# Kernel tuning notes

Hardware: AMD Instinct MI355X
Metric: run time of the kernel (lower is better)

## Reference

```python
import jax, jax.numpy as jnp
import numpy as np
from jax import lax

DN = ('NHWC', 'HWIO', 'NHWC')

def _conv(x, k, b, stride=1):
    return lax.conv_general_dilated(x, k, (stride, stride), 'SAME', dimension_numbers=DN) + b

def _tconv(x, k, b):
    return lax.conv_transpose(x, k, (2, 2), 'SAME', dimension_numbers=DN) + b


def setup_inputs() -> dict:
    key = jax.random.key(0)
    ks = jax.random.split(key, 32)
    ki = iter(ks)
    def w(shape, scale=0.05):
        return (jax.random.normal(next(ki), shape, dtype=jnp.float32) * scale)
    inp = {}
    inp['x'] = jax.random.uniform(next(ki), (8, 128, 128, 3), dtype=jnp.float32)
    # encoder
    inp['k1'],  inp['b1']  = w((11, 11, 3, 32)),   jnp.zeros((32,), jnp.float32)
    inp['k1c'], inp['b1c'] = w((3, 3, 32, 32)),    jnp.zeros((32,), jnp.float32)
    inp['k2'],  inp['b2']  = w((11, 11, 32, 64)),  jnp.zeros((64,), jnp.float32)
    inp['k2c'], inp['b2c'] = w((3, 3, 64, 64)),    jnp.zeros((64,), jnp.float32)
    inp['k3'],  inp['b3']  = w((11, 11, 64, 128)), jnp.zeros((128,), jnp.float32)
    inp['k3c'], inp['b3c'] = w((3, 3, 128, 128)),  jnp.zeros((128,), jnp.float32)
    # codebook (codebookSize=256, latent dim 128)
    inp['codebook'] = w((256, 128), 0.1)
    # decoder
    inp['tk1'],  inp['tb1']  = w((5, 5, 128, 64)), jnp.zeros((64,), jnp.float32)
    inp['tk1c'], inp['tb1c'] = w((3, 3, 64, 64)),  jnp.zeros((64,), jnp.float32)
    inp['tk2'],  inp['tb2']  = w((5, 5, 64, 32)),  jnp.zeros((32,), jnp.float32)
    inp['tk2c'], inp['tb2c'] = w((3, 3, 32, 32)),  jnp.zeros((32,), jnp.float32)
    inp['tk3'],  inp['tb3']  = w((5, 5, 32, 32)),  jnp.zeros((32,), jnp.float32)
    inp['tk3c'], inp['tb3c'] = w((3, 3, 32, 3)),   jnp.zeros((3,), jnp.float32)
    return inp


def reference(x, k1, b1, k1c, b1c, k2, b2, k2c, b2c, k3, b3, k3c, b3c,
              codebook, tk1, tb1, tk1c, tb1c, tk2, tb2, tk2c, tb2c,
              tk3, tb3, tk3c, tb3c):
    act = jax.nn.silu  # flax.nnx.swish
    # encoder
    d1 = act(_conv(x, k1, b1, 2))
    d1 = act(_conv(d1, k1c, b1c, 1))
    d2 = act(_conv(d1, k2, b2, 2))
    d2 = act(_conv(d2, k2c, b2c, 1))
    d3 = act(_conv(d2, k3, b3, 2))
    d3 = _conv(d3, k3c, b3c, 1)               # [B, H/8, W/8, 128]
    # vector quantization: squared L2 to each codebook entry
    lat = d3.reshape(-1, 1, 128)              # [N, 1, 128]
    eu_dis = jnp.sum((lat - codebook[None]) ** 2, axis=-1)   # [N, 256]
    idx = jnp.argmin(eu_dis, axis=-1)         # [N]
    quantized = jnp.take(codebook, idx, axis=0).reshape(d3.shape)
    # straight-through estimator
    replaced = lax.stop_gradient(quantized - d3) + d3
    # decoder
    d4 = act(_tconv(replaced, tk1, tb1))
    d4 = act(_conv(d4, tk1c, tb1c, 1))
    d5 = act(_tconv(d4, tk2, tb2))
    d5 = act(_conv(d5, tk2c, tb2c, 1))
    d6 = act(_tconv(d5, tk3, tb3))
    out = _conv(d6, tk3c, tb3c, 1)            # [B, H, W, 3]
    return out
```

## Files before the change

### kernel.cpp

```cpp
#include <hip/hip_runtime.h>

#define DI __device__ __forceinline__
DI float silu_f(float x){ return x * (1.0f/(1.0f+__expf(-x))); }

template<int X> struct LOG2 { static constexpr int v = 1 + LOG2<X/2>::v; };
template<> struct LOG2<1> { static constexpr int v = 0; };

template<int KH,int KW,int STRIDE,int PAD,int CIN,int COUT,int NPIX,
         bool ACT,bool BIAS,int G,int CS,int TOW>
__global__ __launch_bounds__(256) void conv_k(
    const float* __restrict__ in, const float* __restrict__ w,
    const float* __restrict__ bias, float* __restrict__ out,
    int N,int H,int W,int OH,int OW)
{
  constexpr int CLEN = CIN/G;
  constexpr int COB  = COUT/CS;
  constexpr int COQ  = COB/4;
  constexpr int GSH  = LOG2<G>::v;
  constexpr int CSH  = LOG2<CS>::v;
  constexpr int TAPF = CLEN*COB;
  constexpr bool SALL = (KH*KW*TAPF*4) <= 47*1024;
  constexpr int NTAP = SALL ? KH*KW : KW;
  static_assert(CLEN==3 || (CLEN%4)==0, "ci");
  static_assert(TOW==0 || (!SALL && NPIX==1), "tow");
  __shared__ float sw[NTAP*TAPF];
  constexpr int SPAN = (TOW>0) ? (TOW-1)*STRIDE + KW : 1;
  constexpr int ROWS = (TOW>0) ? (256/COQ)/TOW : 1;
  constexpr int CQ4  = (TOW>0) ? CLEN/4 : 1;
  __shared__ float si[(TOW>0) ? ROWS*CQ4*SPAN*4 : 1];

  const int g  = blockIdx.x & (G-1);
  const int cs = (blockIdx.x >> GSH) & (CS-1);
  const int bx = blockIdx.x >> (GSH+CSH);
  const int total = N*OH*OW;
  if (G>1) out += (size_t)g * total * COUT;
  const int ci_off  = g*CLEN;
  const int co_base = cs*COB;

  int idx = bx*256 + (int)threadIdx.x;
  int cq = idx % COQ;
  int pg = idx / COQ;
  int co = cq*4;
  int gco = co_base + co;
  int p0 = pg*NPIX;

  float acc[NPIX][4] = {};
  int iy0[NPIX], ix0[NPIX]; const float* base[NPIX]; bool pv[NPIX];
#pragma unroll
  for (int t=0;t<NPIX;t++){
    int p=p0+t; pv[t]=(p<total); int pp=pv[t]?p:0;
    int ox=pp%OW; int r=pp/OW; int oy=r%OH; int n=r/OH;
    iy0[t]=oy*STRIDE-PAD; ix0[t]=ox*STRIDE-PAD;
    base[t]=in+(size_t)n*H*W*CIN + ci_off;
  }

  auto stage = [&](int tap0){
    constexpr int TQ = TAPF/4;
    constexpr int V  = NTAP*TQ;
    for (int v=threadIdx.x; v<V; v+=256){
      int tap = v / TQ; int rem = v - tap*TQ;
      float4 q;
      if constexpr (CS==1){
        const float4* src = (const float4*)(w + ((size_t)(tap0+tap)*CIN + ci_off)*COUT);
        q = src[rem];
      } else {
        int ci = rem / (COB/4); int r2 = rem - ci*(COB/4);
        q = *(const float4*)(w + ((size_t)(tap0+tap)*CIN + ci_off + ci)*COUT
                               + co_base + r2*4);
      }
      *(float4*)(sw + (size_t)tap*TAPF + rem*4) = q;
    }
  };

  if constexpr (SALL){
    stage(0);
    __syncthreads();
  }

  if constexpr (TOW>0){
    const int pb0 = bx * (256/COQ);
    const int r0  = pb0 / TOW;
    const int oy0 = r0 % OH;
    const int n0  = r0 / OH;
    const int myrow = (p0 - pb0) / TOW;
    const int oxl   = (p0 - pb0) - myrow*TOW;

    for (int ky=0; ky<KH; ky++){
      __syncthreads();
      stage(ky*KW);
      {
        constexpr int INQ = ROWS*CQ4*SPAN;
        for (int v=(int)threadIdx.x; v<INQ; v+=256){
          int r  = v / (CQ4*SPAN);
          int rm = v - r*(CQ4*SPAN);
          int q  = rm / SPAN;
          int ixo= rm - q*SPAN;
          int iy = (oy0+r)*STRIDE - PAD + ky;
          int ix = ixo - PAD;
          bool ok = iy>=0 && iy<H && ix>=0 && ix<W;
          float4 val = ok ? *(const float4*)(in + ((size_t)(n0*H+iy)*W + ix)*CIN + ci_off + q*4)
                          : make_float4(0.f,0.f,0.f,0.f);
          *(float4*)&si[(size_t)v*4] = val;
        }
      }
      __syncthreads();
      const float* swr = sw;
      for (int kx=0; kx<KW; kx++){
        const float* swt = swr + (size_t)kx*TAPF;
        const int ib = oxl*STRIDE + kx;
#pragma unroll 2
        for (int c=0; c<CQ4; c++){
          float wv[4][4];
#pragma unroll
          for (int r=0;r<4;r++)
            *(float4*)wv[r] = *(const float4*)(swt + (c*4+r)*COB + co);
          float va[4];
          *(float4*)va = *(const float4*)&si[(size_t)((myrow*CQ4 + c)*SPAN + ib)*4];
#pragma unroll
          for (int r=0;r<4;r++)
#pragma unroll
            for (int j=0;j<4;j++)
              acc[0][j]=fmaf(va[r],wv[r][j],acc[0][j]);
        }
      }
    }
  } else {
    for (int ky=0; ky<KH; ky++){
      if constexpr (!SALL){
        __syncthreads();
        stage(ky*KW);
        __syncthreads();
      }
      const float* swr = SALL ? sw + (size_t)ky*KW*TAPF : sw;
      for (int kx=0; kx<KW; kx++){
        const float* swt = swr + (size_t)kx*TAPF;
        const float* ip[NPIX]; bool ok[NPIX];
#pragma unroll
        for (int t=0;t<NPIX;t++){
          int iy=iy0[t]+ky, ix=ix0[t]+kx;
          ok[t]=pv[t] && iy>=0 && iy<H && ix>=0 && ix<W;
          ip[t]=base[t]+(size_t)(iy*W+ix)*CIN;
        }
        if constexpr (CLEN==3){
          float wv[3][4];
          *(float4*)wv[0]=*(const float4*)(swt + 0*COB + co);
          *(float4*)wv[1]=*(const float4*)(swt + 1*COB + co);
          *(float4*)wv[2]=*(const float4*)(swt + 2*COB + co);
#pragma unroll
          for (int t=0;t<NPIX;t++){
            float v0=ok[t]?ip[t][0]:0.f;
            float v1=ok[t]?ip[t][1]:0.f;
            float v2=ok[t]?ip[t][2]:0.f;
#pragma unroll
            for (int j=0;j<4;j++)
              acc[t][j]=fmaf(v0,wv[0][j],fmaf(v1,wv[1][j],fmaf(v2,wv[2][j],acc[t][j])));
          }
        } else {
#pragma unroll 2
          for (int ci=0; ci<CLEN; ci+=4){
            float wv[4][4];
#pragma unroll
            for (int r=0;r<4;r++)
              *(float4*)wv[r] = *(const float4*)(swt + (ci+r)*COB + co);
#pragma unroll
            for (int t=0;t<NPIX;t++){
              float va[4];
              *(float4*)va = ok[t] ? *(const float4*)(ip[t]+ci)
                                   : make_float4(0.f,0.f,0.f,0.f);
#pragma unroll
              for (int r=0;r<4;r++)
#pragma unroll
                for (int j=0;j<4;j++)
                  acc[t][j]=fmaf(va[r],wv[r][j],acc[t][j]);
            }
          }
        }
      }
    }
  }

  float bv[4]={0.f,0.f,0.f,0.f};
  if constexpr (BIAS) *(float4*)bv = *(const float4*)(bias+gco);
#pragma unroll
  for (int t=0;t<NPIX;t++) if (pv[t]){
    float o[4];
#pragma unroll
    for (int j=0;j<4;j++){
      float v = acc[t][j]+bv[j];
      o[j] = ACT ? silu_f(v) : v;
    }
    *(float4*)(out + (size_t)(p0+t)*COUT + gco) = *(float4*)o;
  }
}

template<int G,int COUT,bool ACT>
__global__ __launch_bounds__(256) void reduce_k(
    const float* __restrict__ p, const float* __restrict__ bias,
    float* __restrict__ out, int n)
{
  int i = (blockIdx.x*256+threadIdx.x)*4;
  if (i>=n) return;
  float a[4]; *(float4*)a = *(const float4*)(p+i);
#pragma unroll
  for (int g=1; g<G; g++){
    float b[4]; *(float4*)b = *(const float4*)(p+(size_t)g*n+i);
#pragma unroll
    for (int j=0;j<4;j++) a[j]+=b[j];
  }
  float bv[4]; *(float4*)bv = *(const float4*)(bias + (i % COUT));
#pragma unroll
  for (int j=0;j<4;j++){
    float v=a[j]+bv[j];
    a[j] = ACT ? silu_f(v) : v;
  }
  *(float4*)(out+i) = *(float4*)a;
}

template<int CIN,int COUT,int NPIX,int G,bool DIRECT>
__global__ __launch_bounds__(256) void tconv_k(
    const float* __restrict__ in, const float* __restrict__ w,
    const float* __restrict__ bias, float* __restrict__ out,
    int N,int H,int W,int OH,int OW)
{
  constexpr int COQ  = COUT/4;
  constexpr int CLEN = CIN/G;
  constexpr int GSH  = LOG2<G>::v;
  constexpr int TAPF = CLEN*COUT;
  __shared__ float sw[TAPF];
  const int par = blockIdx.x & 3;
  const int py = par>>1, px = par&1;
  const int g  = (blockIdx.x>>2) & (G-1);
  const int bx = blockIdx.x >> (2+GSH);
  const int NKY = py?3:2, NKX = px?3:2;
  const int OHh=OH>>1, OWh=OW>>1;
  const int total = N*OHh*OWh;
  if (G>1) out += (size_t)g * N*OH*OW*COUT;

  int idx = bx*256 + (int)threadIdx.x;
  int cq = idx % COQ;
  int pg = idx / COQ;
  int co = cq*4;
  int p0 = pg*NPIX;

  float acc[NPIX][4] = {};
  int yy[NPIX], xx[NPIX], nn[NPIX]; const float* base[NPIX]; bool pv[NPIX];
#pragma unroll
  for (int t=0;t<NPIX;t++){
    int p=p0+t; pv[t]=(p<total); int pp=pv[t]?p:0;
    xx[t]=pp%OWh; int r=pp/OWh; yy[t]=r%OHh; nn[t]=r/OHh;
    base[t]=in+(size_t)nn[t]*H*W*CIN + g*CLEN;
  }

  for (int j=0;j<NKY;j++){
    int ky = 2*j + (py?0:1);
    for (int i=0;i<NKX;i++){
      int kx = 2*i + (px?0:1);
      __syncthreads();
      {
        constexpr int V = TAPF/4;
        const float4* src = (const float4*)(w + ((size_t)(ky*5+kx)*CIN + g*CLEN)*COUT);
        for (int v=threadIdx.x; v<V; v+=256) ((float4*)sw)[v]=src[v];
      }
      __syncthreads();
      const float* ip[NPIX]; bool ok[NPIX];
#pragma unroll
      for (int t=0;t<NPIX;t++){
        int iy=yy[t]+j-1, ix=xx[t]+i-1;
        ok[t]=pv[t] && iy>=0 && iy<H && ix>=0 && ix<W;
        ip[t]=base[t]+(size_t)(iy*W+ix)*CIN;
      }
#pragma unroll 2
      for (int ci=0; ci<CLEN; ci+=4){
        float wv[4][4];
#pragma unroll
        for (int r=0;r<4;r++)
          *(float4*)wv[r] = *(const float4*)(sw + (ci+r)*COUT + co);
#pragma unroll
        for (int t=0;t<NPIX;t++){
          float va[4];
          *(float4*)va = ok[t] ? *(const float4*)(ip[t]+ci)
                               : make_float4(0.f,0.f,0.f,0.f);
#pragma unroll
          for (int r=0;r<4;r++)
#pragma unroll
            for (int jj=0;jj<4;jj++)
              acc[t][jj]=fmaf(va[r],wv[r][jj],acc[t][jj]);
        }
      }
    }
  }

  float bv[4]={0.f,0.f,0.f,0.f};
  if constexpr (DIRECT) *(float4*)bv = *(const float4*)(bias+co);
#pragma unroll
  for (int t=0;t<NPIX;t++) if (pv[t]){
    float o[4];
#pragma unroll
    for (int jj=0;jj<4;jj++){
      float v = acc[t][jj]+bv[jj];
      o[jj] = DIRECT ? silu_f(v) : v;
    }
    *(float4*)(out + (((size_t)nn[t]*OH + (2*yy[t]+py))*OW + (2*xx[t]+px))*COUT + co) = *(float4*)o;
  }
}

__global__ __launch_bounds__(256) void vq_k(
    const float* __restrict__ p, const float* __restrict__ bias,
    const float* __restrict__ cb, float* __restrict__ q, int NLat)
{
  __shared__ float slat[4][128];
  int wave = threadIdx.x >> 6;
  int lane = threadIdx.x & 63;
  int l = blockIdx.x*4 + wave;
  if (l >= NLat) return;
  const float* p0 = p + (size_t)l*128;
  const float* p1 = p0 + (size_t)NLat*128;
  slat[wave][lane]    = p0[lane]    + p1[lane]    + bias[lane];
  slat[wave][lane+64] = p0[lane+64] + p1[lane+64] + bias[lane+64];

  float bestd = INFINITY; int besti = 0;
  for (int c0=0;c0<256;c0+=64){
    int c = c0 + lane;
    const float* cp = cb + (size_t)c*128;
    float d = 0.f;
#pragma unroll 8
    for (int k=0;k<128;k+=4){
      float4 cv = *reinterpret_cast<const float4*>(cp+k);
      float d0 = slat[wave][k+0]-cv.x;
      float d1 = slat[wave][k+1]-cv.y;
      float d2 = slat[wave][k+2]-cv.z;
      float d3 = slat[wave][k+3]-cv.w;
      d += d0*d0; d += d1*d1; d += d2*d2; d += d3*d3;
    }
    if (d < bestd) { bestd = d; besti = c; }
  }
  for (int off=32; off; off>>=1){
    float od = __shfl_down(bestd, off);
    int   oi = __shfl_down(besti, off);
    if (od < bestd || (od == bestd && oi < besti)) { bestd=od; besti=oi; }
  }
  besti = __shfl(besti, 0);
  const float* cp = cb + (size_t)besti*128;
  float* qp = q + (size_t)l*128;
  qp[lane]    = cp[lane];
  qp[lane+64] = cp[lane+64];
}

__global__ __launch_bounds__(256) void conv_last_k(
    const float* __restrict__ in, const float* __restrict__ w,
    float* __restrict__ p, int N,int H,int W)
{
  int g = blockIdx.x % 3;
  int bx = blockIdx.x / 3;
  int pix = bx*256 + threadIdx.x;
  int total = N*H*W;
  if (pix>=total) return;
  int x = pix % W; int r = pix / W; int y = r % H; int n = r / H;
  float a0=0.f, a1=0.f, a2=0.f;
  int iy = y + g - 1;
  if (iy>=0 && iy<H){
    const float* base = in + ((size_t)n*H + iy)*W*32;
    for (int kx=0;kx<3;kx++){
      int ix=x+kx-1; if(ix<0||ix>=W) continue;
      const float* ip = base + (size_t)ix*32;
      const float* wp = w + (size_t)((g*3+kx)*32)*3;
#pragma unroll
      for (int ci=0;ci<32;ci+=4){
        float va[4]; *(float4*)va = *(const float4*)(ip+ci);
        float wv[12];
        *(float4*)(wv+0) = *(const float4*)(wp+ci*3+0);
        *(float4*)(wv+4) = *(const float4*)(wp+ci*3+4);
        *(float4*)(wv+8) = *(const float4*)(wp+ci*3+8);
#pragma unroll
        for (int r2=0;r2<4;r2++){
          a0 = fmaf(va[r2], wv[r2*3+0], a0);
          a1 = fmaf(va[r2], wv[r2*3+1], a1);
          a2 = fmaf(va[r2], wv[r2*3+2], a2);
        }
      }
    }
  }
  float* pp = p + (size_t)g*total*3 + (size_t)pix*3;
  pp[0]=a0; pp[1]=a1; pp[2]=a2;
}

__global__ __launch_bounds__(256) void reduce_last_k(
    const float* __restrict__ p, const float* __restrict__ bias,
    float* __restrict__ out, int n)
{
  int i = (blockIdx.x*256+threadIdx.x)*4;
  if (i>=n) return;
  float a[4]; *(float4*)a = *(const float4*)(p+i);
#pragma unroll
  for (int g=1; g<3; g++){
    float b[4]; *(float4*)b = *(const float4*)(p+(size_t)g*n+i);
#pragma unroll
    for (int j=0;j<4;j++) a[j]+=b[j];
  }
  float o[4];
#pragma unroll
  for (int j=0;j<4;j++) o[j] = a[j] + bias[(i+j)%3];
  *(float4*)(out+i) = *(float4*)o;
}

extern "C" void kernel_launch(void* const* d_in, const int* in_sizes, int n_in,
                              void* d_out, int out_size, void* d_ws, size_t ws_size,
                              hipStream_t stream) {
  const float* x    = (const float*)d_in[0];
  const float* k1   = (const float*)d_in[1];  const float* b1  = (const float*)d_in[2];
  const float* k1c  = (const float*)d_in[3];  const float* b1c = (const float*)d_in[4];
  const float* k2   = (const float*)d_in[5];  const float* b2  = (const float*)d_in[6];
  const float* k2c  = (const float*)d_in[7];  const float* b2c = (const float*)d_in[8];
  const float* k3   = (const float*)d_in[9];  const float* b3  = (const float*)d_in[10];
  const float* k3c  = (const float*)d_in[11]; const float* b3c = (const float*)d_in[12];
  const float* cb   = (const float*)d_in[13];
  const float* tk1  = (const float*)d_in[14]; const float* tb1  = (const float*)d_in[15];
  const float* tk1c = (const float*)d_in[16]; const float* tb1c = (const float*)d_in[17];
  const float* tk2  = (const float*)d_in[18]; const float* tb2  = (const float*)d_in[19];
  const float* tk2c = (const float*)d_in[20]; const float* tb2c = (const float*)d_in[21];
  const float* tk3  = (const float*)d_in[22]; const float* tb3  = (const float*)d_in[23];
  const float* tk3c = (const float*)d_in[24]; const float* tb3c = (const float*)d_in[25];
  float* out = (float*)d_out;

  float* S  = (float*)d_ws;
  float* W0 = S;
  float* W1 = S + 1048576;
  float* P  = S + 2097152;
  dim3 blk(256);

  conv_k<11,11,2,4,  3, 32,1,true ,true ,1,2, 0><<<1024,blk,0,stream>>>(x,  k1,  b1,  W0, 8,128,128,64,64);
  conv_k< 3, 3,1,1, 32, 32,1,true ,true ,1,2, 0><<<1024,blk,0,stream>>>(W0, k1c, b1c, W1, 8,64,64,64,64);
  conv_k<11,11,2,4, 32, 64,1,false,false,2,2,32><<<1024,blk,0,stream>>>(W1, k2,  nullptr, P, 8,64,64,32,32);
  reduce_k<2, 64,true><<< 512,blk,0,stream>>>(P, b2,  W0, 524288);
  conv_k< 3, 3,1,1, 64, 64,1,true ,true ,1,2, 0><<< 512,blk,0,stream>>>(W0, k2c, b2c, W1, 8,32,32,32,32);
  conv_k<11,11,2,4, 64,128,1,false,false,4,4,16><<<1024,blk,0,stream>>>(W1, k3,  nullptr, P, 8,32,32,16,16);
  reduce_k<4,128,true><<< 256,blk,0,stream>>>(P, b3,  W0, 262144);
  conv_k< 3, 3,1,1,128,128,1,false,false,2,4, 0><<< 512,blk,0,stream>>>(W0, k3c, nullptr, P, 8,16,16,16,16);
  vq_k<<<512,blk,0,stream>>>(P, b3c, cb, W1, 2048);
  tconv_k<128,64,1,4,false><<<2048,blk,0,stream>>>(W1, tk1, nullptr, P, 8,16,16,32,32);
  reduce_k<4, 64,true><<< 512,blk,0,stream>>>(P, tb1,  W0, 524288);
  conv_k< 3, 3,1,1, 64, 64,1,false,false,2,2, 0><<<1024,blk,0,stream>>>(W0, tk1c, nullptr, P, 8,32,32,32,32);
  reduce_k<2, 64,true><<< 512,blk,0,stream>>>(P, tb1c, W1, 524288);
  tconv_k< 64,32,1,2,false><<<2048,blk,0,stream>>>(W1, tk2, nullptr, P, 8,32,32,64,64);
  reduce_k<2, 32,true><<<1024,blk,0,stream>>>(P, tb2,  W0, 1048576);
  conv_k< 3, 3,1,1, 32, 32,1,true ,true ,1,2, 0><<<1024,blk,0,stream>>>(W0, tk2c, tb2c, W1, 8,64,64,64,64);
  tconv_k< 32,32,2,1,true ><<<2048,blk,0,stream>>>(W1, tk3, tb3, P, 8,64,64,128,128);
  conv_last_k<<<1536,blk,0,stream>>>(P, tk3c, S, 8,128,128);
  reduce_last_k<<<384,blk,0,stream>>>(S, tb3c, out, 393216);
}
```

Baseline: 525.9 us.

## Extend shared-memory input-row tiling to more convolutions, including the 3-channel first layer

Extends the row-tiled convolution path (input rows staged once in shared memory, then reused across output pixels and horizontal taps) to kernels whose full weights fit in shared memory. Adds a special case for the 3-channel first layer. Enables this tiling for the first conv and all 3x3 convs, and switches one 3x3 decoder conv to a 4-way output-channel split. The aim is to cut redundant global or cache loads of overlapping input windows. The cost is an extra sync per kernel row and possible shared-memory bank conflicts from the stride-3 layout.

```diff
diff --git a/kernel.cpp b/kernel.cpp
--- a/kernel.cpp
+++ b/kernel.cpp
@@ -22,12 +22,13 @@
   constexpr bool SALL = (KH*KW*TAPF*4) <= 47*1024;
   constexpr int NTAP = SALL ? KH*KW : KW;
   static_assert(CLEN==3 || (CLEN%4)==0, "ci");
-  static_assert(TOW==0 || (!SALL && NPIX==1), "tow");
+  static_assert(TOW==0 || NPIX==1, "tow");
   __shared__ float sw[NTAP*TAPF];
   constexpr int SPAN = (TOW>0) ? (TOW-1)*STRIDE + KW : 1;
   constexpr int ROWS = (TOW>0) ? (256/COQ)/TOW : 1;
-  constexpr int CQ4  = (TOW>0) ? CLEN/4 : 1;
-  __shared__ float si[(TOW>0) ? ROWS*CQ4*SPAN*4 : 1];
+  constexpr int CQ4  = (TOW>0 && CLEN!=3) ? CLEN/4 : 1;
+  constexpr int SI_F = (TOW==0) ? 1 : (CLEN==3 ? ROWS*SPAN*3 : ROWS*CQ4*SPAN*4);
+  __shared__ float si[SI_F];
 
   const int g  = blockIdx.x & (G-1);
   const int cs = (blockIdx.x >> GSH) & (CS-1);
@@ -55,7 +56,7 @@
   }
 
   auto stage = [&](int tap0){
-    constexpr int TQ = TAPF/4;
+    constexpr int TQ = (CLEN==3) ? (TAPF/4) : (TAPF/4);
     constexpr int V  = NTAP*TQ;
     for (int v=threadIdx.x; v<V; v+=256){
       int tap = v / TQ; int rem = v - tap*TQ;
@@ -63,6 +64,10 @@
       if constexpr (CS==1){
         const float4* src = (const float4*)(w + ((size_t)(tap0+tap)*CIN + ci_off)*COUT);
         q = src[rem];
+      } else if constexpr (CLEN==3){
+        int ci = rem / (COB/4); int r2 = rem - ci*(COB/4);
+        q = *(const float4*)(w + ((size_t)(tap0+tap)*CIN + ci)*COUT
+                               + co_base + r2*4);
       } else {
         int ci = rem / (COB/4); int r2 = rem - ci*(COB/4);
         q = *(const float4*)(w + ((size_t)(tap0+tap)*CIN + ci_off + ci)*COUT
@@ -87,8 +92,21 @@
 
     for (int ky=0; ky<KH; ky++){
       __syncthreads();
-      stage(ky*KW);
-      {
+      if constexpr (!SALL) stage(ky*KW);
+      if constexpr (CLEN==3){
+        constexpr int INS = ROWS*SPAN;
+        for (int v=(int)threadIdx.x; v<INS; v+=256){
+          int r  = v / SPAN;
+          int ixo= v - r*SPAN;
+          int iy = (oy0+r)*STRIDE - PAD + ky;
+          int ix = ixo - PAD;
+          bool ok = iy>=0 && iy<H && ix>=0 && ix<W;
+          const float* ip = in + ((size_t)(n0*H+iy)*W + ix)*CIN;
+          si[v*3+0] = ok?ip[0]:0.f;
+          si[v*3+1] = ok?ip[1]:0.f;
+          si[v*3+2] = ok?ip[2]:0.f;
+        }
+      } else {
         constexpr int INQ = ROWS*CQ4*SPAN;
         for (int v=(int)threadIdx.x; v<INQ; v+=256){
           int r  = v / (CQ4*SPAN);
@@ -104,23 +122,35 @@
         }
       }
       __syncthreads();
-      const float* swr = sw;
+      const float* swr = SALL ? sw + (size_t)ky*KW*TAPF : sw;
       for (int kx=0; kx<KW; kx++){
         const float* swt = swr + (size_t)kx*TAPF;
         const int ib = oxl*STRIDE + kx;
+        if constexpr (CLEN==3){
+          float wv[3][4];
+          *(float4*)wv[0]=*(const float4*)(swt + 0*COB + co);
+          *(float4*)wv[1]=*(const float4*)(swt + 1*COB + co);
+          *(float4*)wv[2]=*(const float4*)(swt + 2*COB + co);
+          const float* sp = &si[(size_t)(myrow*SPAN + ib)*3];
+          float v0=sp[0], v1=sp[1], v2=sp[2];
+#pragma unroll
+          for (int j=0;j<4;j++)
+            acc[0][j]=fmaf(v0,wv[0][j],fmaf(v1,wv[1][j],fmaf(v2,wv[2][j],acc[0][j])));
+        } else {
 #pragma unroll 2
-        for (int c=0; c<CQ4; c++){
-          float wv[4][4];
-#pragma unroll
-          for (int r=0;r<4;r++)
-            *(float4*)wv[r] = *(const float4*)(swt + (c*4+r)*COB + co);
-          float va[4];
-          *(float4*)va = *(const float4*)&si[(size_t)((myrow*CQ4 + c)*SPAN + ib)*4];
-#pragma unroll
-          for (int r=0;r<4;r++)
-#pragma unroll
-            for (int j=0;j<4;j++)
-              acc[0][j]=fmaf(va[r],wv[r][j],acc[0][j]);
+          for (int c=0; c<CQ4; c++){
+            float wv[4][4];
+#pragma unroll
+            for (int r=0;r<4;r++)
+              *(float4*)wv[r] = *(const float4*)(swt + (c*4+r)*COB + co);
+            float va[4];
+            *(float4*)va = *(const float4*)&si[(size_t)((myrow*CQ4 + c)*SPAN + ib)*4];
+#pragma unroll
+            for (int r=0;r<4;r++)
+#pragma unroll
+              for (int j=0;j<4;j++)
+                acc[0][j]=fmaf(va[r],wv[r][j],acc[0][j]);
+          }
         }
       }
     }
@@ -428,22 +458,22 @@
   float* P  = S + 2097152;
   dim3 blk(256);
 
-  conv_k<11,11,2,4,  3, 32,1,true ,true ,1,2, 0><<<1024,blk,0,stream>>>(x,  k1,  b1,  W0, 8,128,128,64,64);
-  conv_k< 3, 3,1,1, 32, 32,1,true ,true ,1,2, 0><<<1024,blk,0,stream>>>(W0, k1c, b1c, W1, 8,64,64,64,64);
+  conv_k<11,11,2,4,  3, 32,1,true ,true ,1,2,64><<<1024,blk,0,stream>>>(x,  k1,  b1,  W0, 8,128,128,64,64);
+  conv_k< 3, 3,1,1, 32, 32,1,true ,true ,1,2,64><<<1024,blk,0,stream>>>(W0, k1c, b1c, W1, 8,64,64,64,64);
   conv_k<11,11,2,4, 32, 64,1,false,false,2,2,32><<<1024,blk,0,stream>>>(W1, k2,  nullptr, P, 8,64,64,32,32);
   reduce_k<2, 64,true><<< 512,blk,0,stream>>>(P, b2,  W0, 524288);
-  conv_k< 3, 3,1,1, 64, 64,1,true ,true ,1,2, 0><<< 512,blk,0,stream>>>(W0, k2c, b2c, W1, 8,32,32,32,32);
+  conv_k< 3, 3,1,1, 64, 64,1,true ,true ,1,2,32><<< 512,blk,0,stream>>>(W0, k2c, b2c, W1, 8,32,32,32,32);
   conv_k<11,11,2,4, 64,128,1,false,false,4,4,16><<<1024,blk,0,stream>>>(W1, k3,  nullptr, P, 8,32,32,16,16);
   reduce_k<4,128,true><<< 256,blk,0,stream>>>(P, b3,  W0, 262144);
-  conv_k< 3, 3,1,1,128,128,1,false,false,2,4, 0><<< 512,blk,0,stream>>>(W0, k3c, nullptr, P, 8,16,16,16,16);
+  conv_k< 3, 3,1,1,128,128,1,false,false,2,4,16><<< 512,blk,0,stream>>>(W0, k3c, nullptr, P, 8,16,16,16,16);
   vq_k<<<512,blk,0,stream>>>(P, b3c, cb, W1, 2048);
   tconv_k<128,64,1,4,false><<<2048,blk,0,stream>>>(W1, tk1, nullptr, P, 8,16,16,32,32);
   reduce_k<4, 64,true><<< 512,blk,0,stream>>>(P, tb1,  W0, 524288);
-  conv_k< 3, 3,1,1, 64, 64,1,false,false,2,2, 0><<<1024,blk,0,stream>>>(W0, tk1c, nullptr, P, 8,32,32,32,32);
+  conv_k< 3, 3,1,1, 64, 64,1,false,false,2,4,32><<<1024,blk,0,stream>>>(W0, tk1c, nullptr, P, 8,32,32,32,32);
   reduce_k<2, 64,true><<< 512,blk,0,stream>>>(P, tb1c, W1, 524288);
   tconv_k< 64,32,1,2,false><<<2048,blk,0,stream>>>(W1, tk2, nullptr, P, 8,32,32,64,64);
   reduce_k<2, 32,true><<<1024,blk,0,stream>>>(P, tb2,  W0, 1048576);
-  conv_k< 3, 3,1,1, 32, 32,1,true ,true ,1,2, 0><<<1024,blk,0,stream>>>(W0, tk2c, tb2c, W1, 8,64,64,64,64);
+  conv_k< 3, 3,1,1, 32, 32,1,true ,true ,1,2,64><<<1024,blk,0,stream>>>(W0, tk2c, tb2c, W1, 8,64,64,64,64);
   tconv_k< 32,32,2,1,true ><<<2048,blk,0,stream>>>(W1, tk3, tb3, P, 8,64,64,128,128);
   conv_last_k<<<1536,blk,0,stream>>>(P, tk3c, S, 8,128,128);
   reduce_last_k<<<384,blk,0,stream>>>(S, tb3c, out, 393216);
```

Result: faster. 496.7 us (-5.6%).
